# Optimization experiments

Hardware: AMD Instinct MI355X
Metric: run time of the kernel (lower is better)

The kernel has to match this reference:

```python
import jax, jax.numpy as jnp
import numpy as np

IN_PLANES = 256
N_POINTS = 262144
N_SEG = 8
BN_EPS = 1e-5


def setup_inputs() -> dict:
    key = jax.random.key(0)
    ks = jax.random.split(key, 8)
    p = jax.random.normal(ks[0], (N_POINTS, 3), dtype=jnp.float32)
    x = jax.random.normal(ks[1], (N_POINTS, IN_PLANES), dtype=jnp.float32)
    # cumulative end-offsets of 8 equal-size point clouds
    o = (jnp.arange(1, N_SEG + 1, dtype=jnp.int32) * (N_POINTS // N_SEG))
    C = IN_PLANES
    s1 = 1.0 / np.sqrt(2 * C)
    s2 = 1.0 / np.sqrt(C)
    W1 = jax.random.uniform(ks[2], (C, 2 * C), jnp.float32, -s1, s1)  # linear1: 2C -> C
    b1 = jax.random.uniform(ks[3], (C,), jnp.float32, -s1, s1)
    gamma1 = jnp.ones((C,), jnp.float32)   # BatchNorm1d affine
    beta1 = jnp.zeros((C,), jnp.float32)
    W2 = jax.random.uniform(ks[4], (C, C), jnp.float32, -s2, s2)      # linear2: C -> C
    b2 = jax.random.uniform(ks[5], (C,), jnp.float32, -s2, s2)
    return {"p": p, "x": x, "o": o, "W1": W1, "b1": b1,
            "gamma1": gamma1, "beta1": beta1, "W2": W2, "b2": b2}


def reference(p, x, o, W1, b1, gamma1, beta1, W2, b2):
    N = x.shape[0]
    B = o.shape[0]
    # segment id of each point from cumulative end-offsets
    seg = jnp.searchsorted(o, jnp.arange(N, dtype=o.dtype), side="right")  # [N]
    counts = (o - jnp.concatenate([jnp.zeros((1,), o.dtype), o[:-1]])).astype(x.dtype)  # [B]
    # per-segment mean (x_b.sum(0)/cnt)
    seg_sum = jax.ops.segment_sum(x, seg, num_segments=B)          # [B, C]
    seg_mean = seg_sum / counts[:, None]
    # linear2 + ReLU on the tiny [B, C] means, then broadcast back to points
    g = jax.nn.relu(seg_mean @ W2.T + b2)                          # [B, C]
    x_cat = jnp.concatenate([x, g[seg]], axis=1)                   # [N, 2C]
    # linear1: Linear -> BatchNorm1d (training stats) -> ReLU
    z = x_cat @ W1.T + b1                                          # [N, C]
    mu = z.mean(axis=0)
    var = z.var(axis=0)  # biased, matches BN training normalization
    z = (z - mu) * jax.lax.rsqrt(var + BN_EPS) * gamma1 + beta1
    return jax.nn.relu(z)
```

## Files before the change

kernel.cpp:

```cpp
#include <hip/hip_runtime.h>
#include <hip/hip_bf16.h>

#define N_PTS  262144
#define CH     256
#define NSEG   8
#define SEGSZ  32768
#define BN_EPS 1e-5f

typedef float  f32x4  __attribute__((ext_vector_type(4)));
typedef __bf16 bf16x8 __attribute__((ext_vector_type(8)));
typedef unsigned short u16x8 __attribute__((ext_vector_type(8)));

__global__ void prep_w(const float* __restrict__ W1,
                       unsigned short* __restrict__ Whi,
                       unsigned short* __restrict__ Wlo) {
    int i = (blockIdx.x * 256 + threadIdx.x) * 4;
    #pragma unroll
    for (int e = 0; e < 4; ++e) {
        int idx = i + e;
        int c = idx >> 8, k = idx & 255;
        float v = W1[c * 512 + k];
        __bf16 hb = (__bf16)v;
        __bf16 lb = (__bf16)(v - (float)hb);
        Whi[idx] = __builtin_bit_cast(unsigned short, hb);
        Wlo[idx] = __builtin_bit_cast(unsigned short, lb);
    }
}

#define BM 128
#define BK 64

__global__ __launch_bounds__(512) void
gemm_stats(const float* __restrict__ x,
           const unsigned short* __restrict__ Whi,
           const unsigned short* __restrict__ Wlo,
           float* __restrict__ zA,
           float* __restrict__ part_x,
           float* __restrict__ part_zs,
           float* __restrict__ part_zq) {
    __shared__ char smem[96 * 1024];
    __shared__ float segx_lds[8][CH];

    const int tid  = threadIdx.x;
    const int lane = tid & 63;
    const int wv   = tid >> 6;
    const int wr   = wv >> 2;
    const int wc   = wv & 3;
    const int blockRow = blockIdx.x * BM;

    f32x4 acc[4][4] = {};

    const int ar = lane & 15;
    const int kg = lane >> 4;

    for (int ks = 0; ks < 4; ++ks) {
        const int kwin = ks * 64;
        __syncthreads();

        float xs[8];
        #pragma unroll
        for (int e = 0; e < 8; ++e) xs[e] = 0.f;
        {
            const int r0 = tid >> 3;
            const int cg = tid & 7;
            #pragma unroll
            for (int p = 0; p < 2; ++p) {
                int r = p * 64 + r0;
                const float* src = x + (size_t)(blockRow + r) * CH + kwin + cg * 8;
                f32x4 v0 = *(const f32x4*)(src);
                f32x4 v1 = *(const f32x4*)(src + 4);
                float vv[8];
                #pragma unroll
                for (int e = 0; e < 4; ++e) { vv[e] = v0[e]; vv[4 + e] = v1[e]; }
                u16x8 hv, lv;
                #pragma unroll
                for (int e = 0; e < 8; ++e) {
                    xs[e] += vv[e];
                    __bf16 hb = (__bf16)vv[e];
                    __bf16 lb = (__bf16)(vv[e] - (float)hb);
                    hv[e] = __builtin_bit_cast(unsigned short, hb);
                    lv[e] = __builtin_bit_cast(unsigned short, lb);
                }
                int off = r * 128 + ((cg * 16) ^ ((r & 7) << 4));
                *(u16x8*)(smem + off)         = hv;
                *(u16x8*)(smem + 16384 + off) = lv;
            }
            #pragma unroll
            for (int p = 0; p < 4; ++p) {
                int c = p * 64 + r0;
                u16x8 hv = *(const u16x8*)(Whi + c * 256 + kwin + cg * 8);
                u16x8 lv = *(const u16x8*)(Wlo + c * 256 + kwin + cg * 8);
                int off = c * 128 + ((cg * 16) ^ ((c & 7) << 4));
                *(u16x8*)(smem + 32768 + off) = hv;
                *(u16x8*)(smem + 65536 + off) = lv;
            }
        }
        #pragma unroll
        for (int m = 8; m <= 32; m <<= 1)
            #pragma unroll
            for (int e = 0; e < 8; ++e) xs[e] += __shfl_xor(xs[e], m);
        if (lane < 8) {
            #pragma unroll
            for (int e = 0; e < 8; ++e)
                segx_lds[wv][kwin + lane * 8 + e] = xs[e];
        }
        __syncthreads();

        #pragma unroll
        for (int kk = 0; kk < 2; ++kk) {
            const int kb = kk * 64 + kg * 16;
            bf16x8 bh[4], bl[4];
            #pragma unroll
            for (int n = 0; n < 4; ++n) {
                int rb = wc * 64 + n * 16 + ar;
                int off = rb * 128 + (kb ^ ((rb & 7) << 4));
                bh[n] = *(const bf16x8*)(smem + 32768 + off);
                bl[n] = *(const bf16x8*)(smem + 65536 + off);
            }
            #pragma unroll
            for (int m = 0; m < 4; ++m) {
                int ra = wr * 64 + m * 16 + ar;
                int off = ra * 128 + (kb ^ ((ra & 7) << 4));
                bf16x8 ah = *(const bf16x8*)(smem + off);
                bf16x8 al = *(const bf16x8*)(smem + 16384 + off);
                #pragma unroll
                for (int n = 0; n < 4; ++n) {
                    acc[m][n] = __builtin_amdgcn_mfma_f32_16x16x32_bf16(ah, bh[n], acc[m][n], 0, 0, 0);
                    acc[m][n] = __builtin_amdgcn_mfma_f32_16x16x32_bf16(ah, bl[n], acc[m][n], 0, 0, 0);
                    acc[m][n] = __builtin_amdgcn_mfma_f32_16x16x32_bf16(al, bh[n], acc[m][n], 0, 0, 0);
                }
            }
        }
    }

    const int rg = lane >> 4;
    #pragma unroll
    for (int m = 0; m < 4; ++m)
        #pragma unroll
        for (int j = 0; j < 4; ++j) {
            int row = blockRow + wr * 64 + m * 16 + rg * 4 + j;
            float* dst = zA + (size_t)row * CH + wc * 64 + (lane & 15);
            #pragma unroll
            for (int n = 0; n < 4; ++n) dst[n * 16] = acc[m][n][j];
        }

    __syncthreads();
    float* zs_lds = (float*)smem;
    float* zq_lds = (float*)(smem + 2048);
    #pragma unroll
    for (int n = 0; n < 4; ++n) {
        float s = 0.f, q = 0.f;
        #pragma unroll
        for (int m = 0; m < 4; ++m)
            #pragma unroll
            for (int j = 0; j < 4; ++j) { float v = acc[m][n][j]; s += v; q += v * v; }
        s += __shfl_xor(s, 16); s += __shfl_xor(s, 32);
        q += __shfl_xor(q, 16); q += __shfl_xor(q, 32);
        if (lane < 16) {
            int col = wc * 64 + n * 16 + lane;
            zs_lds[wr * CH + col] = s;
            zq_lds[wr * CH + col] = q;
        }
    }
    __syncthreads();
    if (tid < CH) {
        float sx = 0.f;
        #pragma unroll
        for (int w = 0; w < 8; ++w) sx += segx_lds[w][tid];
        const size_t o = (size_t)blockIdx.x * CH + tid;
        part_x [o] = sx;
        part_zs[o] = zs_lds[tid] + zs_lds[CH + tid];
        part_zq[o] = zq_lds[tid] + zq_lds[CH + tid];
    }
}

__global__ __launch_bounds__(256) void
reduce_parts(const float* __restrict__ part_x, const float* __restrict__ part_zs,
             const float* __restrict__ part_zq, float* __restrict__ mid_x,
             float* __restrict__ mid_zs, float* __restrict__ mid_zq) {
    const int c = threadIdx.x;
    const int base = blockIdx.x * 32;
    float sx = 0.f, ss = 0.f, sq = 0.f;
    for (int r = 0; r < 32; ++r) {
        size_t idx = (size_t)(base + r) * CH + c;
        sx += part_x[idx]; ss += part_zs[idx]; sq += part_zq[idx];
    }
    mid_x [blockIdx.x * CH + c] = sx;
    mid_zs[blockIdx.x * CH + c] = ss;
    mid_zq[blockIdx.x * CH + c] = sq;
}

__global__ void finalize(const float* __restrict__ mid_x,
                         const float* __restrict__ mid_zs,
                         const float* __restrict__ mid_zq,
                         const float* __restrict__ W1, const float* __restrict__ b1,
                         const float* __restrict__ gamma1, const float* __restrict__ beta1,
                         const float* __restrict__ W2, const float* __restrict__ b2,
                         float* __restrict__ scale, float* __restrict__ off) {
    __shared__ float sm[NSEG][CH];
    __shared__ float gl[NSEG][CH];
    const int c = threadIdx.x;
    float zseg[NSEG];
    for (int b = 0; b < NSEG; ++b) {
        float a = 0.f, d = 0.f;
        #pragma unroll
        for (int s = 0; s < 8; ++s) {
            a += mid_x [(b * 8 + s) * CH + c];
            d += mid_zs[(b * 8 + s) * CH + c];
        }
        sm[b][c] = a * (1.f / SEGSZ);
        zseg[b] = d;
    }
    float zq = 0.f;
    for (int i = 0; i < 64; ++i) zq += mid_zq[i * CH + c];
    __syncthreads();
    float g[NSEG];
    #pragma unroll
    for (int b = 0; b < NSEG; ++b) g[b] = b2[c];
    for (int k = 0; k < CH; ++k) {
        float w = W2[c * CH + k];
        #pragma unroll
        for (int b = 0; b < NSEG; ++b) g[b] += sm[b][k] * w;
    }
    for (int b = 0; b < NSEG; ++b) gl[b][c] = fmaxf(g[b], 0.f);
    __syncthreads();
    float h[NSEG];
    #pragma unroll
    for (int b = 0; b < NSEG; ++b) h[b] = b1[c];
    for (int k = 0; k < CH; ++k) {
        float w = W1[c * 512 + 256 + k];
        #pragma unroll
        for (int b = 0; b < NSEG; ++b) h[b] += gl[b][k] * w;
    }
    float S1 = 0.f, sh = 0.f, cross = 0.f, sh2 = 0.f;
    #pragma unroll
    for (int b = 0; b < NSEG; ++b) {
        S1 += zseg[b]; sh += h[b]; cross += h[b] * zseg[b]; sh2 += h[b] * h[b];
    }
    const float Nf = (float)N_PTS;
    float mu  = (S1 + (float)SEGSZ * sh) / Nf;
    float SS  = zq + 2.f * cross + (float)SEGSZ * sh2;
    float var = SS / Nf - mu * mu;
    float sc  = gamma1[c] * rsqrtf(var + BN_EPS);
    scale[c] = sc;
    for (int b = 0; b < NSEG; ++b) off[b * CH + c] = (h[b] - mu) * sc + beta1[c];
}

__global__ __launch_bounds__(256) void
apply_bn(float* __restrict__ z, const float* __restrict__ scale,
         const float* __restrict__ off) {
    const int total = N_PTS * (CH / 4);
    f32x4* z4 = (f32x4*)z;
    int idx = blockIdx.x * blockDim.x + threadIdx.x;
    int stride = gridDim.x * blockDim.x;
    for (int f = idx; f < total; f += stride) {
        int i  = f >> 6;
        int c4 = (f & 63) << 2;
        int sg = i >> 15;
        f32x4 v = z4[f];
        f32x4 s = *(const f32x4*)(scale + c4);
        f32x4 o = *(const f32x4*)(off + sg * CH + c4);
        #pragma unroll
        for (int e = 0; e < 4; ++e) v[e] = fmaxf(v[e] * s[e] + o[e], 0.f);
        z4[f] = v;
    }
}

extern "C" void kernel_launch(void* const* d_in, const int* in_sizes, int n_in,
                              void* d_out, int out_size, void* d_ws, size_t ws_size,
                              hipStream_t stream) {
    const float* x      = (const float*)d_in[1];
    const float* W1     = (const float*)d_in[3];
    const float* b1     = (const float*)d_in[4];
    const float* gamma1 = (const float*)d_in[5];
    const float* beta1  = (const float*)d_in[6];
    const float* W2     = (const float*)d_in[7];
    const float* b2     = (const float*)d_in[8];
    float* out = (float*)d_out;
    char*  ws  = (char*)d_ws;
    float* part_x  = (float*)(ws);
    float* part_zs = (float*)(ws + (size_t)(2u << 20));
    float* part_zq = (float*)(ws + (size_t)(4u << 20));
    char*  tail    = ws + (size_t)(6u << 20);
    float* mid_x   = (float*)(tail);
    float* mid_zs  = (float*)(tail + 65536);
    float* mid_zq  = (float*)(tail + 131072);
    float* scale   = (float*)(tail + 196608);
    float* off     = (float*)(tail + 197632);
    unsigned short* Whi = (unsigned short*)(tail + 262144);
    unsigned short* Wlo = (unsigned short*)(tail + 262144 + 131072);

    prep_w<<<64, 256, 0, stream>>>(W1, Whi, Wlo);
    gemm_stats<<<N_PTS / BM, 512, 0, stream>>>(x, Whi, Wlo, out,
                                               part_x, part_zs, part_zq);
    reduce_parts<<<64, 256, 0, stream>>>(part_x, part_zs, part_zq,
                                         mid_x, mid_zs, mid_zq);
    finalize<<<1, 256, 0, stream>>>(mid_x, mid_zs, mid_zq,
                                    W1, b1, gamma1, beta1, W2, b2, scale, off);
    apply_bn<<<2048, 256, 0, stream>>>(out, scale, off);
}
```

Measured before the change: 660.6 us.

## Halve GEMM LDS footprint via two-pass weight tiles, split finalize across segments

The GEMM kernel now stages the W1 hi/lo tiles in two 128-column halves and reuses one 32KB LDS region, dropping shared memory from 96KB to 64KB, and it sets a min-blocks launch bound to raise occupancy. The cost is two extra barriers and a second weight load per k-step. The single-block finalize kernel is split into an 8-block per-segment MLP kernel plus a small BN-stats kernel, which spreads the serial 256x256 matvec work across more CUs. The apply_bn grid is doubled. Together these target latency hiding in the main GEMM and the serial tail.

```diff
diff --git a/kernel.cpp b/kernel.cpp
--- a/kernel.cpp
+++ b/kernel.cpp
@@ -30,7 +30,7 @@
 #define BM 128
 #define BK 64
 
-__global__ __launch_bounds__(512) void
+__global__ __launch_bounds__(512, 4) void
 gemm_stats(const float* __restrict__ x,
            const unsigned short* __restrict__ Whi,
            const unsigned short* __restrict__ Wlo,
@@ -38,7 +38,7 @@
            float* __restrict__ part_x,
            float* __restrict__ part_zs,
            float* __restrict__ part_zq) {
-    __shared__ char smem[96 * 1024];
+    __shared__ char smem[64 * 1024];
     __shared__ float segx_lds[8][CH];
 
     const int tid  = threadIdx.x;
@@ -85,15 +85,16 @@
                 *(u16x8*)(smem + off)         = hv;
                 *(u16x8*)(smem + 16384 + off) = lv;
             }
-            #pragma unroll
-            for (int p = 0; p < 4; ++p) {
-                int c = p * 64 + r0;
-                u16x8 hv = *(const u16x8*)(Whi + c * 256 + kwin + cg * 8);
-                u16x8 lv = *(const u16x8*)(Wlo + c * 256 + kwin + cg * 8);
-                int off = c * 128 + ((cg * 16) ^ ((c & 7) << 4));
-                *(u16x8*)(smem + 32768 + off) = hv;
-                *(u16x8*)(smem + 65536 + off) = lv;
-            }
+        }
+        #pragma unroll
+        for (int j = 0; j < 2; ++j) {
+            int chunk = j * 512 + tid;
+            int row = chunk >> 3, cgb = chunk & 7;
+            u16x8 hv = *(const u16x8*)(Whi + row * 256 + kwin + cgb * 8);
+            u16x8 lv = *(const u16x8*)(Wlo + row * 256 + kwin + cgb * 8);
+            int offb = row * 128 + ((cgb * 16) ^ ((row & 7) << 4));
+            *(u16x8*)(smem + 32768 + offb) = hv;
+            *(u16x8*)(smem + 49152 + offb) = lv;
         }
         #pragma unroll
         for (int m = 8; m <= 32; m <<= 1)
@@ -109,13 +110,13 @@
         #pragma unroll
         for (int kk = 0; kk < 2; ++kk) {
             const int kb = kk * 64 + kg * 16;
-            bf16x8 bh[4], bl[4];
-            #pragma unroll
-            for (int n = 0; n < 4; ++n) {
-                int rb = wc * 64 + n * 16 + ar;
-                int off = rb * 128 + (kb ^ ((rb & 7) << 4));
-                bh[n] = *(const bf16x8*)(smem + 32768 + off);
-                bl[n] = *(const bf16x8*)(smem + 65536 + off);
+            bf16x8 bh[2], bl[2];
+            #pragma unroll
+            for (int n = 0; n < 2; ++n) {
+                int rbl = wc * 32 + n * 16 + ar;
+                int offb = rbl * 128 + (kb ^ ((rbl & 7) << 4));
+                bh[n] = *(const bf16x8*)(smem + 32768 + offb);
+                bl[n] = *(const bf16x8*)(smem + 49152 + offb);
             }
             #pragma unroll
             for (int m = 0; m < 4; ++m) {
@@ -124,42 +125,83 @@
                 bf16x8 ah = *(const bf16x8*)(smem + off);
                 bf16x8 al = *(const bf16x8*)(smem + 16384 + off);
                 #pragma unroll
-                for (int n = 0; n < 4; ++n) {
+                for (int n = 0; n < 2; ++n) {
                     acc[m][n] = __builtin_amdgcn_mfma_f32_16x16x32_bf16(ah, bh[n], acc[m][n], 0, 0, 0);
                     acc[m][n] = __builtin_amdgcn_mfma_f32_16x16x32_bf16(ah, bl[n], acc[m][n], 0, 0, 0);
                     acc[m][n] = __builtin_amdgcn_mfma_f32_16x16x32_bf16(al, bh[n], acc[m][n], 0, 0, 0);
                 }
             }
         }
+        __syncthreads();
+
+        #pragma unroll
+        for (int j = 0; j < 2; ++j) {
+            int chunk = j * 512 + tid;
+            int row = chunk >> 3, cgb = chunk & 7;
+            u16x8 hv = *(const u16x8*)(Whi + (128 + row) * 256 + kwin + cgb * 8);
+            u16x8 lv = *(const u16x8*)(Wlo + (128 + row) * 256 + kwin + cgb * 8);
+            int offb = row * 128 + ((cgb * 16) ^ ((row & 7) << 4));
+            *(u16x8*)(smem + 32768 + offb) = hv;
+            *(u16x8*)(smem + 49152 + offb) = lv;
+        }
+        __syncthreads();
+
+        #pragma unroll
+        for (int kk = 0; kk < 2; ++kk) {
+            const int kb = kk * 64 + kg * 16;
+            bf16x8 bh[2], bl[2];
+            #pragma unroll
+            for (int n = 0; n < 2; ++n) {
+                int rbl = wc * 32 + n * 16 + ar;
+                int offb = rbl * 128 + (kb ^ ((rbl & 7) << 4));
+                bh[n] = *(const bf16x8*)(smem + 32768 + offb);
+                bl[n] = *(const bf16x8*)(smem + 49152 + offb);
+            }
+            #pragma unroll
+            for (int m = 0; m < 4; ++m) {
+                int ra = wr * 64 + m * 16 + ar;
+                int off = ra * 128 + (kb ^ ((ra & 7) << 4));
+                bf16x8 ah = *(const bf16x8*)(smem + off);
+                bf16x8 al = *(const bf16x8*)(smem + 16384 + off);
+                #pragma unroll
+                for (int n = 0; n < 2; ++n) {
+                    acc[m][2 + n] = __builtin_amdgcn_mfma_f32_16x16x32_bf16(ah, bh[n], acc[m][2 + n], 0, 0, 0);
+                    acc[m][2 + n] = __builtin_amdgcn_mfma_f32_16x16x32_bf16(ah, bl[n], acc[m][2 + n], 0, 0, 0);
+                    acc[m][2 + n] = __builtin_amdgcn_mfma_f32_16x16x32_bf16(al, bh[n], acc[m][2 + n], 0, 0, 0);
+                }
+            }
+        }
     }
 
     const int rg = lane >> 4;
+    const int cbase = wc * 32 + (lane & 15);
     #pragma unroll
     for (int m = 0; m < 4; ++m)
         #pragma unroll
         for (int j = 0; j < 4; ++j) {
             int row = blockRow + wr * 64 + m * 16 + rg * 4 + j;
-            float* dst = zA + (size_t)row * CH + wc * 64 + (lane & 15);
-            #pragma unroll
-            for (int n = 0; n < 4; ++n) dst[n * 16] = acc[m][n][j];
+            float* dst = zA + (size_t)row * CH;
+            #pragma unroll
+            for (int q = 0; q < 4; ++q)
+                dst[(q >> 1) * 128 + (q & 1) * 16 + cbase] = acc[m][q][j];
         }
 
     __syncthreads();
     float* zs_lds = (float*)smem;
     float* zq_lds = (float*)(smem + 2048);
     #pragma unroll
-    for (int n = 0; n < 4; ++n) {
-        float s = 0.f, q = 0.f;
+    for (int q = 0; q < 4; ++q) {
+        float s = 0.f, qq = 0.f;
         #pragma unroll
         for (int m = 0; m < 4; ++m)
             #pragma unroll
-            for (int j = 0; j < 4; ++j) { float v = acc[m][n][j]; s += v; q += v * v; }
+            for (int j = 0; j < 4; ++j) { float v = acc[m][q][j]; s += v; qq += v * v; }
         s += __shfl_xor(s, 16); s += __shfl_xor(s, 32);
-        q += __shfl_xor(q, 16); q += __shfl_xor(q, 32);
+        qq += __shfl_xor(qq, 16); qq += __shfl_xor(qq, 32);
         if (lane < 16) {
-            int col = wc * 64 + n * 16 + lane;
+            int col = (q >> 1) * 128 + wc * 32 + (q & 1) * 16 + lane;
             zs_lds[wr * CH + col] = s;
-            zq_lds[wr * CH + col] = q;
+            zq_lds[wr * CH + col] = qq;
         }
     }
     __syncthreads();
@@ -190,52 +232,53 @@
     mid_zq[blockIdx.x * CH + c] = sq;
 }
 
-__global__ void finalize(const float* __restrict__ mid_x,
-                         const float* __restrict__ mid_zs,
+__global__ __launch_bounds__(256) void
+seg_mlp(const float* __restrict__ mid_x, const float* __restrict__ mid_zs,
+        const float* __restrict__ W1, const float* __restrict__ b1,
+        const float* __restrict__ W2, const float* __restrict__ b2,
+        float* __restrict__ hseg, float* __restrict__ zseg) {
+    __shared__ float sm[CH];
+    __shared__ float gl[CH];
+    const int b = blockIdx.x;
+    const int c = threadIdx.x;
+    float a = 0.f, d = 0.f;
+    #pragma unroll
+    for (int s = 0; s < 8; ++s) {
+        a += mid_x [(b * 8 + s) * CH + c];
+        d += mid_zs[(b * 8 + s) * CH + c];
+    }
+    sm[c] = a * (1.f / SEGSZ);
+    zseg[b * CH + c] = d;
+    __syncthreads();
+    float g = b2[c];
+    for (int k = 0; k < CH; k += 4) {
+        f32x4 w = *(const f32x4*)(W2 + c * CH + k);
+        g += sm[k] * w[0] + sm[k + 1] * w[1] + sm[k + 2] * w[2] + sm[k + 3] * w[3];
+    }
+    gl[c] = fmaxf(g, 0.f);
+    __syncthreads();
+    float h = b1[c];
+    for (int k = 0; k < CH; k += 4) {
+        f32x4 w = *(const f32x4*)(W1 + c * 512 + 256 + k);
+        h += gl[k] * w[0] + gl[k + 1] * w[1] + gl[k + 2] * w[2] + gl[k + 3] * w[3];
+    }
+    hseg[b * CH + c] = h;
+}
+
+__global__ void bn_final(const float* __restrict__ hseg, const float* __restrict__ zseg,
                          const float* __restrict__ mid_zq,
-                         const float* __restrict__ W1, const float* __restrict__ b1,
                          const float* __restrict__ gamma1, const float* __restrict__ beta1,
-                         const float* __restrict__ W2, const float* __restrict__ b2,
                          float* __restrict__ scale, float* __restrict__ off) {
-    __shared__ float sm[NSEG][CH];
-    __shared__ float gl[NSEG][CH];
     const int c = threadIdx.x;
-    float zseg[NSEG];
-    for (int b = 0; b < NSEG; ++b) {
-        float a = 0.f, d = 0.f;
-        #pragma unroll
-        for (int s = 0; s < 8; ++s) {
-            a += mid_x [(b * 8 + s) * CH + c];
-            d += mid_zs[(b * 8 + s) * CH + c];
-        }
-        sm[b][c] = a * (1.f / SEGSZ);
-        zseg[b] = d;
-    }
     float zq = 0.f;
     for (int i = 0; i < 64; ++i) zq += mid_zq[i * CH + c];
-    __syncthreads();
-    float g[NSEG];
-    #pragma unroll
-    for (int b = 0; b < NSEG; ++b) g[b] = b2[c];
-    for (int k = 0; k < CH; ++k) {
-        float w = W2[c * CH + k];
-        #pragma unroll
-        for (int b = 0; b < NSEG; ++b) g[b] += sm[b][k] * w;
-    }
-    for (int b = 0; b < NSEG; ++b) gl[b][c] = fmaxf(g[b], 0.f);
-    __syncthreads();
+    float S1 = 0.f, sh = 0.f, cross = 0.f, sh2 = 0.f;
     float h[NSEG];
     #pragma unroll
-    for (int b = 0; b < NSEG; ++b) h[b] = b1[c];
-    for (int k = 0; k < CH; ++k) {
-        float w = W1[c * 512 + 256 + k];
-        #pragma unroll
-        for (int b = 0; b < NSEG; ++b) h[b] += gl[b][k] * w;
-    }
-    float S1 = 0.f, sh = 0.f, cross = 0.f, sh2 = 0.f;
-    #pragma unroll
     for (int b = 0; b < NSEG; ++b) {
-        S1 += zseg[b]; sh += h[b]; cross += h[b] * zseg[b]; sh2 += h[b] * h[b];
+        h[b] = hseg[b * CH + c];
+        float zs = zseg[b * CH + c];
+        S1 += zs; sh += h[b]; cross += h[b] * zs; sh2 += h[b] * h[b];
     }
     const float Nf = (float)N_PTS;
     float mu  = (S1 + (float)SEGSZ * sh) / Nf;
@@ -243,6 +286,7 @@
     float var = SS / Nf - mu * mu;
     float sc  = gamma1[c] * rsqrtf(var + BN_EPS);
     scale[c] = sc;
+    #pragma unroll
     for (int b = 0; b < NSEG; ++b) off[b * CH + c] = (h[b] - mu) * sc + beta1[c];
 }
 
@@ -287,6 +331,8 @@
     float* mid_zq  = (float*)(tail + 131072);
     float* scale   = (float*)(tail + 196608);
     float* off     = (float*)(tail + 197632);
+    float* hseg    = (float*)(tail + 205824);
+    float* zseg    = (float*)(tail + 214016);
     unsigned short* Whi = (unsigned short*)(tail + 262144);
     unsigned short* Wlo = (unsigned short*)(tail + 262144 + 131072);
 
@@ -295,7 +341,7 @@
                                                part_x, part_zs, part_zq);
     reduce_parts<<<64, 256, 0, stream>>>(part_x, part_zs, part_zq,
                                          mid_x, mid_zs, mid_zq);
-    finalize<<<1, 256, 0, stream>>>(mid_x, mid_zs, mid_zq,
-                                    W1, b1, gamma1, beta1, W2, b2, scale, off);
-    apply_bn<<<2048, 256, 0, stream>>>(out, scale, off);
-}
+    seg_mlp<<<NSEG, 256, 0, stream>>>(mid_x, mid_zs, W1, b1, W2, b2, hseg, zseg);
+    bn_final<<<1, 256, 0, stream>>>(hseg, zseg, mid_zq, gamma1, beta1, scale, off);
+    apply_bn<<<4096, 256, 0, stream>>>(out, scale, off);
+}
```

New measurement: 646.0 us. 2.2% less time.

## Prefetch GEMM tiles into registers with double-buffered LDS and fuse the reduction tail

Applied to the files above, without the earlier changes.

The GEMM now loads the next K-window of x and of the split-bf16 weights into registers while MFMAs run on the current window. A-tiles are double-buffered in a 128KB LDS arena to hide global-load latency, and a barrier per iteration is removed. The partial reduce and the single-block finalize are replaced by an 8-block per-segment reduce+MLP kernel. apply_bn now recomputes scale and offset into shared memory per block, which cuts one launch and a serial single-block stage. The larger LDS footprint and extra registers may limit occupancy.

```diff
diff --git a/kernel.cpp b/kernel.cpp
--- a/kernel.cpp
+++ b/kernel.cpp
@@ -28,9 +28,8 @@
 }
 
 #define BM 128
-#define BK 64
-
-__global__ __launch_bounds__(512) void
+
+__global__ __launch_bounds__(512, 2) void
 gemm_stats(const float* __restrict__ x,
            const unsigned short* __restrict__ Whi,
            const unsigned short* __restrict__ Wlo,
@@ -38,7 +37,7 @@
            float* __restrict__ part_x,
            float* __restrict__ part_zs,
            float* __restrict__ part_zq) {
-    __shared__ char smem[96 * 1024];
+    __shared__ char smem[128 * 1024];
     __shared__ float segx_lds[8][CH];
 
     const int tid  = threadIdx.x;
@@ -52,48 +51,51 @@
 
     const int ar = lane & 15;
     const int kg = lane >> 4;
-
-    for (int ks = 0; ks < 4; ++ks) {
-        const int kwin = ks * 64;
-        __syncthreads();
-
+    const int r0 = tid >> 3;
+    const int cg = tid & 7;
+
+    f32x4 pa[2][2];
+    u16x8 pbh[4], pbl[4];
+
+    auto loadA = [&](int kwin) {
+        #pragma unroll
+        for (int p = 0; p < 2; ++p) {
+            const float* src = x + (size_t)(blockRow + p * 64 + r0) * CH + kwin + cg * 8;
+            pa[p][0] = *(const f32x4*)(src);
+            pa[p][1] = *(const f32x4*)(src + 4);
+        }
+    };
+    auto loadB = [&](int kwin) {
+        #pragma unroll
+        for (int j = 0; j < 4; ++j) {
+            int chunk = j * 512 + tid;
+            int row = chunk >> 3, cgb = chunk & 7;
+            pbh[j] = *(const u16x8*)(Whi + row * 256 + kwin + cgb * 8);
+            pbl[j] = *(const u16x8*)(Wlo + row * 256 + kwin + cgb * 8);
+        }
+    };
+    auto stageA = [&](int buf, int kwin) {
         float xs[8];
         #pragma unroll
         for (int e = 0; e < 8; ++e) xs[e] = 0.f;
-        {
-            const int r0 = tid >> 3;
-            const int cg = tid & 7;
-            #pragma unroll
-            for (int p = 0; p < 2; ++p) {
-                int r = p * 64 + r0;
-                const float* src = x + (size_t)(blockRow + r) * CH + kwin + cg * 8;
-                f32x4 v0 = *(const f32x4*)(src);
-                f32x4 v1 = *(const f32x4*)(src + 4);
-                float vv[8];
-                #pragma unroll
-                for (int e = 0; e < 4; ++e) { vv[e] = v0[e]; vv[4 + e] = v1[e]; }
-                u16x8 hv, lv;
-                #pragma unroll
-                for (int e = 0; e < 8; ++e) {
-                    xs[e] += vv[e];
-                    __bf16 hb = (__bf16)vv[e];
-                    __bf16 lb = (__bf16)(vv[e] - (float)hb);
-                    hv[e] = __builtin_bit_cast(unsigned short, hb);
-                    lv[e] = __builtin_bit_cast(unsigned short, lb);
-                }
-                int off = r * 128 + ((cg * 16) ^ ((r & 7) << 4));
-                *(u16x8*)(smem + off)         = hv;
-                *(u16x8*)(smem + 16384 + off) = lv;
+        #pragma unroll
+        for (int p = 0; p < 2; ++p) {
+            float vv[8];
+            #pragma unroll
+            for (int e = 0; e < 4; ++e) { vv[e] = pa[p][0][e]; vv[4 + e] = pa[p][1][e]; }
+            u16x8 hv, lv;
+            #pragma unroll
+            for (int e = 0; e < 8; ++e) {
+                xs[e] += vv[e];
+                __bf16 hb = (__bf16)vv[e];
+                __bf16 lb = (__bf16)(vv[e] - (float)hb);
+                hv[e] = __builtin_bit_cast(unsigned short, hb);
+                lv[e] = __builtin_bit_cast(unsigned short, lb);
             }
-            #pragma unroll
-            for (int p = 0; p < 4; ++p) {
-                int c = p * 64 + r0;
-                u16x8 hv = *(const u16x8*)(Whi + c * 256 + kwin + cg * 8);
-                u16x8 lv = *(const u16x8*)(Wlo + c * 256 + kwin + cg * 8);
-                int off = c * 128 + ((cg * 16) ^ ((c & 7) << 4));
-                *(u16x8*)(smem + 32768 + off) = hv;
-                *(u16x8*)(smem + 65536 + off) = lv;
-            }
+            int r = p * 64 + r0;
+            int off = buf * 32768 + r * 128 + ((cg * 16) ^ ((r0 & 7) << 4));
+            *(u16x8*)(smem + off)         = hv;
+            *(u16x8*)(smem + 16384 + off) = lv;
         }
         #pragma unroll
         for (int m = 8; m <= 32; m <<= 1)
@@ -104,7 +106,25 @@
             for (int e = 0; e < 8; ++e)
                 segx_lds[wv][kwin + lane * 8 + e] = xs[e];
         }
-        __syncthreads();
+    };
+    auto stageB = [&]() {
+        #pragma unroll
+        for (int j = 0; j < 4; ++j) {
+            int chunk = j * 512 + tid;
+            int row = chunk >> 3, cgb = chunk & 7;
+            int offb = row * 128 + ((cgb * 16) ^ ((row & 7) << 4));
+            *(u16x8*)(smem + 65536 + offb) = pbh[j];
+            *(u16x8*)(smem + 98304 + offb) = pbl[j];
+        }
+    };
+
+    loadA(0); loadB(0);
+    stageA(0, 0); stageB();
+    __syncthreads();
+
+    for (int ks = 0; ks < 4; ++ks) {
+        const int cur = ks & 1;
+        if (ks < 3) { loadA((ks + 1) * 64); loadB((ks + 1) * 64); }
 
         #pragma unroll
         for (int kk = 0; kk < 2; ++kk) {
@@ -113,16 +133,16 @@
             #pragma unroll
             for (int n = 0; n < 4; ++n) {
                 int rb = wc * 64 + n * 16 + ar;
-                int off = rb * 128 + (kb ^ ((rb & 7) << 4));
-                bh[n] = *(const bf16x8*)(smem + 32768 + off);
-                bl[n] = *(const bf16x8*)(smem + 65536 + off);
+                int offb = rb * 128 + (kb ^ ((rb & 7) << 4));
+                bh[n] = *(const bf16x8*)(smem + 65536 + offb);
+                bl[n] = *(const bf16x8*)(smem + 98304 + offb);
             }
             #pragma unroll
             for (int m = 0; m < 4; ++m) {
                 int ra = wr * 64 + m * 16 + ar;
-                int off = ra * 128 + (kb ^ ((ra & 7) << 4));
-                bf16x8 ah = *(const bf16x8*)(smem + off);
-                bf16x8 al = *(const bf16x8*)(smem + 16384 + off);
+                int offa = cur * 32768 + ra * 128 + (kb ^ ((ra & 7) << 4));
+                bf16x8 ah = *(const bf16x8*)(smem + offa);
+                bf16x8 al = *(const bf16x8*)(smem + 16384 + offa);
                 #pragma unroll
                 for (int n = 0; n < 4; ++n) {
                     acc[m][n] = __builtin_amdgcn_mfma_f32_16x16x32_bf16(ah, bh[n], acc[m][n], 0, 0, 0);
@@ -131,6 +151,12 @@
                 }
             }
         }
+        __syncthreads();
+        if (ks < 3) {
+            stageA(cur ^ 1, (ks + 1) * 64);
+            stageB();
+            __syncthreads();
+        }
     }
 
     const int rg = lane >> 4;
@@ -144,7 +170,6 @@
             for (int n = 0; n < 4; ++n) dst[n * 16] = acc[m][n][j];
         }
 
-    __syncthreads();
     float* zs_lds = (float*)smem;
     float* zq_lds = (float*)(smem + 2048);
     #pragma unroll
@@ -174,81 +199,85 @@
     }
 }
 
+__global__ __launch_bounds__(1024) void
+seg_reduce_mlp(const float* __restrict__ part_x, const float* __restrict__ part_zs,
+               const float* __restrict__ part_zq,
+               const float* __restrict__ W1, const float* __restrict__ b1,
+               const float* __restrict__ W2, const float* __restrict__ b2,
+               float* __restrict__ hseg, float* __restrict__ zseg,
+               float* __restrict__ zqseg) {
+    __shared__ float red[3][4][CH];
+    __shared__ float sm[CH];
+    __shared__ float gl[CH];
+    const int tid = threadIdx.x;
+    const int c = tid & 255;
+    const int q = tid >> 8;
+    const int b = blockIdx.x;
+    float sx = 0.f, ss = 0.f, sq = 0.f;
+    const int rbase = b * 256 + q * 64;
+    #pragma unroll 4
+    for (int r = 0; r < 64; ++r) {
+        size_t idx = (size_t)(rbase + r) * CH + c;
+        sx += part_x[idx]; ss += part_zs[idx]; sq += part_zq[idx];
+    }
+    red[0][q][c] = sx; red[1][q][c] = ss; red[2][q][c] = sq;
+    __syncthreads();
+    if (q == 0) {
+        sx = red[0][0][c] + red[0][1][c] + red[0][2][c] + red[0][3][c];
+        ss = red[1][0][c] + red[1][1][c] + red[1][2][c] + red[1][3][c];
+        sq = red[2][0][c] + red[2][1][c] + red[2][2][c] + red[2][3][c];
+        zseg [b * CH + c] = ss;
+        zqseg[b * CH + c] = sq;
+        sm[c] = sx * (1.f / SEGSZ);
+    }
+    __syncthreads();
+    if (q == 0) {
+        float g = b2[c];
+        for (int k = 0; k < CH; k += 4) {
+            f32x4 w = *(const f32x4*)(W2 + c * CH + k);
+            g += sm[k] * w[0] + sm[k + 1] * w[1] + sm[k + 2] * w[2] + sm[k + 3] * w[3];
+        }
+        gl[c] = fmaxf(g, 0.f);
+    }
+    __syncthreads();
+    if (q == 0) {
+        float h = b1[c];
+        for (int k = 0; k < CH; k += 4) {
+            f32x4 w = *(const f32x4*)(W1 + c * 512 + 256 + k);
+            h += gl[k] * w[0] + gl[k + 1] * w[1] + gl[k + 2] * w[2] + gl[k + 3] * w[3];
+        }
+        hseg[b * CH + c] = h;
+    }
+}
+
 __global__ __launch_bounds__(256) void
-reduce_parts(const float* __restrict__ part_x, const float* __restrict__ part_zs,
-             const float* __restrict__ part_zq, float* __restrict__ mid_x,
-             float* __restrict__ mid_zs, float* __restrict__ mid_zq) {
-    const int c = threadIdx.x;
-    const int base = blockIdx.x * 32;
-    float sx = 0.f, ss = 0.f, sq = 0.f;
-    for (int r = 0; r < 32; ++r) {
-        size_t idx = (size_t)(base + r) * CH + c;
-        sx += part_x[idx]; ss += part_zs[idx]; sq += part_zq[idx];
-    }
-    mid_x [blockIdx.x * CH + c] = sx;
-    mid_zs[blockIdx.x * CH + c] = ss;
-    mid_zq[blockIdx.x * CH + c] = sq;
-}
-
-__global__ void finalize(const float* __restrict__ mid_x,
-                         const float* __restrict__ mid_zs,
-                         const float* __restrict__ mid_zq,
-                         const float* __restrict__ W1, const float* __restrict__ b1,
-                         const float* __restrict__ gamma1, const float* __restrict__ beta1,
-                         const float* __restrict__ W2, const float* __restrict__ b2,
-                         float* __restrict__ scale, float* __restrict__ off) {
-    __shared__ float sm[NSEG][CH];
-    __shared__ float gl[NSEG][CH];
-    const int c = threadIdx.x;
-    float zseg[NSEG];
-    for (int b = 0; b < NSEG; ++b) {
-        float a = 0.f, d = 0.f;
-        #pragma unroll
-        for (int s = 0; s < 8; ++s) {
-            a += mid_x [(b * 8 + s) * CH + c];
-            d += mid_zs[(b * 8 + s) * CH + c];
-        }
-        sm[b][c] = a * (1.f / SEGSZ);
-        zseg[b] = d;
-    }
-    float zq = 0.f;
-    for (int i = 0; i < 64; ++i) zq += mid_zq[i * CH + c];
-    __syncthreads();
-    float g[NSEG];
-    #pragma unroll
-    for (int b = 0; b < NSEG; ++b) g[b] = b2[c];
-    for (int k = 0; k < CH; ++k) {
-        float w = W2[c * CH + k];
-        #pragma unroll
-        for (int b = 0; b < NSEG; ++b) g[b] += sm[b][k] * w;
-    }
-    for (int b = 0; b < NSEG; ++b) gl[b][c] = fmaxf(g[b], 0.f);
-    __syncthreads();
-    float h[NSEG];
-    #pragma unroll
-    for (int b = 0; b < NSEG; ++b) h[b] = b1[c];
-    for (int k = 0; k < CH; ++k) {
-        float w = W1[c * 512 + 256 + k];
-        #pragma unroll
-        for (int b = 0; b < NSEG; ++b) h[b] += gl[b][k] * w;
-    }
-    float S1 = 0.f, sh = 0.f, cross = 0.f, sh2 = 0.f;
-    #pragma unroll
-    for (int b = 0; b < NSEG; ++b) {
-        S1 += zseg[b]; sh += h[b]; cross += h[b] * zseg[b]; sh2 += h[b] * h[b];
-    }
-    const float Nf = (float)N_PTS;
-    float mu  = (S1 + (float)SEGSZ * sh) / Nf;
-    float SS  = zq + 2.f * cross + (float)SEGSZ * sh2;
-    float var = SS / Nf - mu * mu;
-    float sc  = gamma1[c] * rsqrtf(var + BN_EPS);
-    scale[c] = sc;
-    for (int b = 0; b < NSEG; ++b) off[b * CH + c] = (h[b] - mu) * sc + beta1[c];
-}
-
-__global__ __launch_bounds__(256) void
-apply_bn(float* __restrict__ z, const float* __restrict__ scale,
-         const float* __restrict__ off) {
+apply_bn(float* __restrict__ z,
+         const float* __restrict__ hseg, const float* __restrict__ zseg,
+         const float* __restrict__ zqseg,
+         const float* __restrict__ gamma1, const float* __restrict__ beta1) {
+    __shared__ float s_scale[CH];
+    __shared__ float s_off[NSEG][CH];
+    {
+        const int c = threadIdx.x;
+        float zq = 0.f, S1 = 0.f, sh = 0.f, cross = 0.f, sh2 = 0.f;
+        float h[NSEG];
+        #pragma unroll
+        for (int b = 0; b < NSEG; ++b) {
+            h[b] = hseg[b * CH + c];
+            float zs = zseg[b * CH + c];
+            zq += zqseg[b * CH + c];
+            S1 += zs; sh += h[b]; cross += h[b] * zs; sh2 += h[b] * h[b];
+        }
+        const float Nf = (float)N_PTS;
+        float mu  = (S1 + (float)SEGSZ * sh) / Nf;
+        float SS  = zq + 2.f * cross + (float)SEGSZ * sh2;
+        float var = SS / Nf - mu * mu;
+        float sc  = gamma1[c] * rsqrtf(var + BN_EPS);
+        s_scale[c] = sc;
+        #pragma unroll
+        for (int b = 0; b < NSEG; ++b) s_off[b][c] = (h[b] - mu) * sc + beta1[c];
+    }
+    __syncthreads();
     const int total = N_PTS * (CH / 4);
     f32x4* z4 = (f32x4*)z;
     int idx = blockIdx.x * blockDim.x + threadIdx.x;
@@ -258,8 +287,8 @@
         int c4 = (f & 63) << 2;
         int sg = i >> 15;
         f32x4 v = z4[f];
-        f32x4 s = *(const f32x4*)(scale + c4);
-        f32x4 o = *(const f32x4*)(off + sg * CH + c4);
+        f32x4 s = *(const f32x4*)(&s_scale[c4]);
+        f32x4 o = *(const f32x4*)(&s_off[sg][c4]);
         #pragma unroll
         for (int e = 0; e < 4; ++e) v[e] = fmaxf(v[e] * s[e] + o[e], 0.f);
         z4[f] = v;
@@ -282,20 +311,16 @@
     float* part_zs = (float*)(ws + (size_t)(2u << 20));
     float* part_zq = (float*)(ws + (size_t)(4u << 20));
     char*  tail    = ws + (size_t)(6u << 20);
-    float* mid_x   = (float*)(tail);
-    float* mid_zs  = (float*)(tail + 65536);
-    float* mid_zq  = (float*)(tail + 131072);
-    float* scale   = (float*)(tail + 196608);
-    float* off     = (float*)(tail + 197632);
-    unsigned short* Whi = (unsigned short*)(tail + 262144);
-    unsigned short* Wlo = (unsigned short*)(tail + 262144 + 131072);
+    float* hseg    = (float*)(tail);
+    float* zseg    = (float*)(tail + 8192);
+    float* zqseg   = (float*)(tail + 16384);
+    unsigned short* Whi = (unsigned short*)(tail + 32768);
+    unsigned short* Wlo = (unsigned short*)(tail + 32768 + 131072);
 
     prep_w<<<64, 256, 0, stream>>>(W1, Whi, Wlo);
     gemm_stats<<<N_PTS / BM, 512, 0, stream>>>(x, Whi, Wlo, out,
                                                part_x, part_zs, part_zq);
-    reduce_parts<<<64, 256, 0, stream>>>(part_x, part_zs, part_zq,
-                                         mid_x, mid_zs, mid_zq);
-    finalize<<<1, 256, 0, stream>>>(mid_x, mid_zs, mid_zq,
-                                    W1, b1, gamma1, beta1, W2, b2, scale, off);
-    apply_bn<<<2048, 256, 0, stream>>>(out, scale, off);
-}
+    seg_reduce_mlp<<<NSEG, 1024, 0, stream>>>(part_x, part_zs, part_zq,
+                                              W1, b1, W2, b2, hseg, zseg, zqseg);
+    apply_bn<<<4096, 256, 0, stream>>>(out, hseg, zseg, zqseg, gamma1, beta1);
+}
```

Measured after the change: 617.9 us. -6.5%, faster.
